# Performance work log

Hardware: AMD Instinct MI355X
Metric: run time of the kernel (lower is better)

The kernel has to match this reference:

```python
import jax, jax.numpy as jnp
import numpy as np

N_NODES = 50000
N_EDGES = 800000
N_REL = 16
N_GRAPHS = 64
IN_DIM = 128
HID = 128
FC = 256
N_CLASSES = 16


def setup_inputs() -> dict:
    key = jax.random.key(0)
    ks = jax.random.split(key, 16)
    h = jax.random.normal(ks[0], (N_NODES, IN_DIM), dtype=jnp.float32)
    src = jax.random.randint(ks[1], (N_EDGES,), 0, N_NODES, dtype=jnp.int32)
    dst = jax.random.randint(ks[2], (N_EDGES,), 0, N_NODES, dtype=jnp.int32)
    rel_types = jax.random.randint(ks[3], (N_EDGES,), 0, N_REL, dtype=jnp.int32)
    graph_ids = jnp.sort(jax.random.randint(ks[4], (N_NODES,), 0, N_GRAPHS, dtype=jnp.int32))
    s1 = 1.0 / np.sqrt(IN_DIM)
    s2 = 1.0 / np.sqrt(HID)
    # RGCN layer 1: per-relation weights, self-loop weight, bias
    W1 = jax.random.normal(ks[5], (N_REL, IN_DIM, HID), dtype=jnp.float32) * s1
    Ws1 = jax.random.normal(ks[6], (IN_DIM, HID), dtype=jnp.float32) * s1
    b1 = jnp.zeros((HID,), dtype=jnp.float32)
    # RGCN layer 2
    W2 = jax.random.normal(ks[7], (N_REL, HID, HID), dtype=jnp.float32) * s2
    Ws2 = jax.random.normal(ks[8], (HID, HID), dtype=jnp.float32) * s2
    b2 = jnp.zeros((HID,), dtype=jnp.float32)
    # FC layer after mean pooling
    Wfc = jax.random.normal(ks[9], (HID, FC), dtype=jnp.float32) * s2
    bfc = jnp.zeros((FC,), dtype=jnp.float32)
    # classify head
    Wc = jax.random.normal(ks[10], (FC, N_CLASSES), dtype=jnp.float32) * (1.0 / np.sqrt(FC))
    bc = jnp.zeros((N_CLASSES,), dtype=jnp.float32)
    return dict(h=h, src=src, dst=dst, rel_types=rel_types, graph_ids=graph_ids,
                W1=W1, Ws1=Ws1, b1=b1, W2=W2, Ws2=Ws2, b2=b2,
                Wfc=Wfc, bfc=bfc, Wc=Wc, bc=bc)


def _rel_graph_conv(h, W, Ws, b, src, dst, rel):
    # dgl RelGraphConv (regularizer=None, self_loop=True, bias=True):
    # out[v] = sum_{e:(u->v)} W[rel_e] @ h[u] + Ws @ h[v] + b
    hW = jnp.einsum('ni,rio->rno', h, W)            # [R, N, out]
    msg = hW[rel, src]                               # [E, out] gather per edge
    agg = jax.ops.segment_sum(msg, dst, num_segments=N_NODES)
    return agg + h @ Ws + b


def _mean_nodes(h, graph_ids):
    sums = jax.ops.segment_sum(h, graph_ids, num_segments=N_GRAPHS)      # [G, D]
    cnts = jax.ops.segment_sum(jnp.ones((h.shape[0], 1), h.dtype), graph_ids,
                               num_segments=N_GRAPHS)                    # [G, 1]
    return sums / jnp.maximum(cnts, 1.0)


def reference(h, src, dst, rel_types, graph_ids,
              W1, Ws1, b1, W2, Ws2, b2, Wfc, bfc, Wc, bc):
    h = h.astype(jnp.float32)
    h = jax.nn.relu(_rel_graph_conv(h, W1, Ws1, b1, src, dst, rel_types))
    h = jax.nn.relu(_rel_graph_conv(h, W2, Ws2, b2, src, dst, rel_types))
    hg = _mean_nodes(h, graph_ids)                   # [G, HID]
    hg = jax.nn.relu(hg @ Wfc + bfc)                 # [G, FC]
    return jax.nn.softmax(hg @ Wc + bc, axis=1)      # [G, n_classes]
```

## Files before the change

kernel.cpp:

```cpp
#include <hip/hip_runtime.h>
#include <hip/hip_bf16.h>

#define N_NODES   50000
#define N_PAD     50048
#define N_EDGES   800000
#define N_REL     16
#define N_GRAPHS  64
#define DIM       128
#define FC_DIM    256
#define N_CLASSES 16

#define SB        50176
#define NBINS_P   (16 * SB)
#define NBLK_PP   784
#define NCOARSE   782
#define NCH       98
#define CHSZ      8192
#define POOL_CH   64
#define MAXBLK_A  13294

#define WS_MARK   0
#define WS_HG     802816
#define WS_CNT    835584
#define WS_SRCOF  835840
#define MEMSET_SZ 4038912
#define WS_BLKH   4038912
#define WS_COFS   4345600
#define WS_PARTP  4348928
#define WS_BLKB   4352256
#define WS_RELB   4355584
#define WS_CIDMAP 4355840
#define WS_RTMP   7567104
#define WS_RECS   10767104
#define WS_OFFSD  13967104
#define WS_X1     14167552
#define WS_X2     26979840
#define WS_AGG    39792128
#define WS_WB     52604416
#define WS_T      53718528

#define XW_TOTAL  (N_PAD * DIM + 2 * 17 * 16384)

typedef __attribute__((ext_vector_type(8))) short bf16x8;
typedef __attribute__((ext_vector_type(4))) float f32x4;

__device__ __forceinline__ void atomAddF(float* p, float v) {
#if defined(__gfx90a__) || defined(__gfx942__) || defined(__gfx950__)
    unsafeAtomicAdd(p, v);
#else
    atomicAdd(p, v);
#endif
}

__device__ __forceinline__ float bf2f(unsigned int u) {
    union { float f; unsigned int i; } x; x.i = u << 16; return x.f;
}
__device__ __forceinline__ unsigned short f2bf(float f) {
    union { float f; unsigned int u; } x; x.f = f;
    unsigned int r = x.u + 0x7fff + ((x.u >> 16) & 1);
    return (unsigned short)(r >> 16);
}
__device__ __forceinline__ void accum8(float* qa, uint4 u) {
    qa[0] += bf2f(u.x & 0xffff); qa[1] += bf2f(u.x >> 16);
    qa[2] += bf2f(u.y & 0xffff); qa[3] += bf2f(u.y >> 16);
    qa[4] += bf2f(u.z & 0xffff); qa[5] += bf2f(u.z >> 16);
    qa[6] += bf2f(u.w & 0xffff); qa[7] += bf2f(u.w >> 16);
}
__device__ __forceinline__ void pack16(const float* qa, unsigned short* dst) {
    #pragma unroll
    for (int j = 0; j < 2; ++j) {
        uint4 w;
        w.x = ((unsigned int)f2bf(qa[j*8+1]) << 16) | f2bf(qa[j*8+0]);
        w.y = ((unsigned int)f2bf(qa[j*8+3]) << 16) | f2bf(qa[j*8+2]);
        w.z = ((unsigned int)f2bf(qa[j*8+5]) << 16) | f2bf(qa[j*8+4]);
        w.w = ((unsigned int)f2bf(qa[j*8+7]) << 16) | f2bf(qa[j*8+6]);
        ((uint4*)dst)[j] = w;
    }
}

__global__ void k_convXW(const float* __restrict__ h, unsigned short* __restrict__ x1,
                         const float* __restrict__ W1, const float* __restrict__ Ws1,
                         const float* __restrict__ W2, const float* __restrict__ Ws2,
                         unsigned short* __restrict__ Wb) {
    int id = blockIdx.x * blockDim.x + threadIdx.x;
    if (id < N_PAD * DIM) {
        int v = id >> 7;
        x1[id] = (v < N_NODES) ? f2bf(h[id]) : (unsigned short)0;
    } else {
        int t = id - N_PAD * DIM;
        int l = t / 278528, rem = t % 278528;
        int r = rem >> 14, rr = rem & 16383;
        int n = rr >> 7, k = rr & 127;
        const float* W  = l ? W2 : W1;
        const float* Ws = l ? Ws2 : Ws1;
        float v = (r < 16) ? W[r * 16384 + k * 128 + n] : Ws[k * 128 + n];
        Wb[t] = f2bf(v);
    }
}

__global__ __launch_bounds__(256) void k_h1(
    const int* __restrict__ src, const int* __restrict__ dst, const int* __restrict__ rel,
    unsigned char* __restrict__ mark, int* __restrict__ blockHist)
{
    __shared__ int hl[NCOARSE];
    int b = blockIdx.x, t = threadIdx.x;
    for (int i = t; i < NCOARSE; i += 256) hl[i] = 0;
    __syncthreads();
    int e0 = b * CHSZ;
    int eend = min(e0 + CHSZ, N_EDGES);
    for (int e = e0 + t; e < eend; e += 256) {
        int d = dst[e];
        mark[rel[e] * SB + src[e]] = 1;
        atomicAdd(&hl[d >> 6], 1);
    }
    __syncthreads();
    for (int i = t; i < NCOARSE; i += 256) blockHist[b * NCOARSE + i] = hl[i];
}

__global__ void k_cscan(int* __restrict__ blockHist, int* __restrict__ coarseOffs) {
    __shared__ int s1[1024], s2[1024];
    int t = threadIdx.x;
    int tot = 0;
    if (t < NCOARSE) {
        int run = 0;
        for (int b = 0; b < NCH; ++b) {
            int v = blockHist[b * NCOARSE + t];
            blockHist[b * NCOARSE + t] = run;
            run += v;
        }
        tot = run;
    }
    s1[t] = tot; __syncthreads();
    int* cur = s1; int* nxt = s2;
    for (int o = 1; o < 1024; o <<= 1) {
        nxt[t] = cur[t] + ((t >= o) ? cur[t - o] : 0);
        __syncthreads();
        int* tmp = cur; cur = nxt; nxt = tmp;
    }
    if (t < NCOARSE) {
        int base = cur[t] - tot;
        coarseOffs[t] = base;
        for (int b = 0; b < NCH; ++b) blockHist[b * NCOARSE + t] += base;
    }
    if (t == NCOARSE) coarseOffs[NCOARSE] = cur[NCOARSE - 1];
}

__global__ void k_scanPA(const unsigned int* __restrict__ markU, int* __restrict__ partP) {
    __shared__ int red[256];
    int b = blockIdx.x, t = threadIdx.x;
    unsigned int u = markU[b * 256 + t];
    red[t] = (int)((u & 1) + ((u >> 8) & 1) + ((u >> 16) & 1) + ((u >> 24) & 1));
    __syncthreads();
    for (int o = 128; o > 0; o >>= 1) {
        if (t < o) red[t] += red[t + o];
        __syncthreads();
    }
    if (t == 0) partP[b] = red[0];
}

__global__ void k_scanPB(const int* __restrict__ partP, int* __restrict__ blkB,
                         int* __restrict__ relB) {
    __shared__ int s1[784], s2[784];
    __shared__ int tot[16], rbase[17];
    int t = threadIdx.x;
    int rel = t / 49, pos = t - rel * 49;
    int v = (t < 784) ? partP[t] : 0;
    if (t < 784) s1[t] = v;
    __syncthreads();
    int* cur = s1; int* nxt = s2;
    for (int o = 1; o < 64; o <<= 1) {
        if (t < 784) nxt[t] = cur[t] + ((pos >= o) ? cur[t - o] : 0);
        __syncthreads();
        int* tmp = cur; cur = nxt; nxt = tmp;
    }
    if (t < 784 && pos == 48) tot[rel] = cur[t];
    __syncthreads();
    if (t == 0) {
        int base = 0;
        for (int r = 0; r < 16; ++r) { rbase[r] = base; base += (tot[r] + 63) & ~63; }
        rbase[16] = base;
    }
    __syncthreads();
    if (t < 784) blkB[t] = rbase[rel] + cur[t] - v;
    if (t < 17)  relB[t] = rbase[t];
}

__global__ void k_scanPC(const unsigned int* __restrict__ markU, const int* __restrict__ blkB,
                         int* __restrict__ cidMap, int* __restrict__ srcOf) {
    __shared__ int s1[256], s2[256];
    int b = blockIdx.x, t = threadIdx.x;
    unsigned int u = markU[b * 256 + t];
    int f0 = (int)(u & 1), f1 = (int)((u >> 8) & 1);
    int f2 = (int)((u >> 16) & 1), f3 = (int)((u >> 24) & 1);
    int sum = f0 + f1 + f2 + f3;
    s1[t] = sum; __syncthreads();
    int* cur = s1; int* nxt = s2;
    for (int o = 1; o < 256; o <<= 1) {
        nxt[t] = cur[t] + ((t >= o) ? cur[t - o] : 0);
        __syncthreads();
        int* tmp = cur; cur = nxt; nxt = tmp;
    }
    int cid = blkB[b] + cur[t] - sum;
    int rel = b / 49;
    int key0 = b * 1024 + t * 4;
    int srcBase = key0 - rel * SB;
    if (f0) { cidMap[key0]     = cid; srcOf[cid] = srcBase;     cid++; }
    if (f1) { cidMap[key0 + 1] = cid; srcOf[cid] = srcBase + 1; cid++; }
    if (f2) { cidMap[key0 + 2] = cid; srcOf[cid] = srcBase + 2; cid++; }
    if (f3) { cidMap[key0 + 3] = cid; srcOf[cid] = srcBase + 3; cid++; }
}

__global__ __launch_bounds__(256) void k_scat1(
    const int* __restrict__ src, const int* __restrict__ dst, const int* __restrict__ rel,
    const int* __restrict__ cidMap, const int* __restrict__ blockHist,
    unsigned int* __restrict__ rtmp)
{
    __shared__ int baseL[NCOARSE];
    __shared__ int hl[NCOARSE];
    int b = blockIdx.x, t = threadIdx.x;
    for (int i = t; i < NCOARSE; i += 256) { baseL[i] = blockHist[b * NCOARSE + i]; hl[i] = 0; }
    __syncthreads();
    int e0 = b * CHSZ;
    int eend = min(e0 + CHSZ, N_EDGES);
    for (int e = e0 + t; e < eend; e += 256) {
        int d = dst[e];
        int cid = cidMap[rel[e] * SB + src[e]];
        int c = d >> 6;
        int rank = atomicAdd(&hl[c], 1);
        rtmp[baseL[c] + rank] = ((unsigned int)cid << 6) | (unsigned int)(d & 63);
    }
}

__global__ __launch_bounds__(256) void k_p2(
    const unsigned int* __restrict__ rtmp, const int* __restrict__ coarseOffs,
    unsigned int* __restrict__ recs, int* __restrict__ offsD)
{
    __shared__ int cntL[64], exclL[65], cur2[64];
    int i = blockIdx.x, t = threadIdx.x;
    int segB = coarseOffs[i], segE = coarseOffs[i + 1];
    if (t < 64) { cntL[t] = 0; cur2[t] = 0; }
    __syncthreads();
    for (int e = segB + t; e < segE; e += 256)
        atomicAdd(&cntL[rtmp[e] & 63u], 1);
    __syncthreads();
    if (t == 0) {
        int run = segB;
        #pragma unroll
        for (int d = 0; d < 64; ++d) { exclL[d] = run; run += cntL[d]; }
        exclL[64] = run;
    }
    __syncthreads();
    if (t < 64) offsD[i * 64 + t] = exclL[t];
    if (t == 64) offsD[i * 64 + 64] = exclL[64];
    for (int e = segB + t; e < segE; e += 256) {
        unsigned int r = rtmp[e];
        int d = (int)(r & 63u);
        int rank = atomicAdd(&cur2[d], 1);
        recs[exclL[d] + rank] = r >> 6;
    }
}

__global__ __launch_bounds__(256) void k_phaseA(
    const unsigned short* __restrict__ x, const unsigned short* __restrict__ Wb,
    const int* __restrict__ srcOf, const int* __restrict__ relB,
    unsigned short* __restrict__ T)
{
    __shared__ unsigned short S[64 * 136];
    __shared__ int sSrc[64];
    __shared__ int sRB[17];

    int tid = threadIdx.x;
    if (tid < 17) sRB[tid] = relB[tid];
    __syncthreads();

    int row0 = blockIdx.x * 64;
    int rtot = sRB[16];
    if (row0 >= rtot + N_PAD) return;

    int r = 16;
    #pragma unroll
    for (int i = 0; i < 16; ++i)
        if (row0 < sRB[i + 1]) { r = i; break; }

    if (tid < 64) sSrc[tid] = (r == 16) ? (row0 - rtot + tid) : srcOf[row0 + tid];
    __syncthreads();

    {
        int row = tid >> 2, c0 = tid & 3;
        const uint4* xp = (const uint4*)(x + (size_t)sSrc[row] * DIM);
        uint4* lp = (uint4*)(&S[row * 136]);
        #pragma unroll
        for (int i = 0; i < 4; ++i) lp[c0 + 4 * i] = xp[c0 + 4 * i];
    }
    __syncthreads();

    int w = tid >> 6, l = tid & 63;
    int nl = l & 15, q = l >> 4;

    f32x4 acc[4][2];
    #pragma unroll
    for (int m = 0; m < 4; ++m) {
        acc[m][0] = (f32x4){0.f, 0.f, 0.f, 0.f};
        acc[m][1] = (f32x4){0.f, 0.f, 0.f, 0.f};
    }

    const unsigned short* wr = Wb + r * 16384;
    #pragma unroll
    for (int kc = 0; kc < 4; ++kc) {
        bf16x8 B0 = *(const bf16x8*)(wr + (w * 32 + nl) * 128 + kc * 32 + q * 8);
        bf16x8 B1 = *(const bf16x8*)(wr + (w * 32 + 16 + nl) * 128 + kc * 32 + q * 8);
        #pragma unroll
        for (int m = 0; m < 4; ++m) {
            bf16x8 a = *(const bf16x8*)(&S[(m * 16 + nl) * 136 + kc * 32 + q * 8]);
            acc[m][0] = __builtin_amdgcn_mfma_f32_16x16x32_bf16(B0, a, acc[m][0], 0, 0, 0);
            acc[m][1] = __builtin_amdgcn_mfma_f32_16x16x32_bf16(B1, a, acc[m][1], 0, 0, 0);
        }
    }
    __syncthreads();
    #pragma unroll
    for (int m = 0; m < 4; ++m) {
        #pragma unroll
        for (int nt = 0; nt < 2; ++nt) {
            uint2 wv;
            wv.x = ((unsigned int)f2bf(acc[m][nt][1]) << 16) | f2bf(acc[m][nt][0]);
            wv.y = ((unsigned int)f2bf(acc[m][nt][3]) << 16) | f2bf(acc[m][nt][2]);
            *(uint2*)(&S[(m * 16 + nl) * 136 + w * 32 + nt * 16 + q * 4]) = wv;
        }
    }
    __syncthreads();
    {
        unsigned short* Tb = T + (size_t)row0 * DIM;
        #pragma unroll
        for (int it = 0; it < 4; ++it) {
            int c = tid + it * 256;
            int row = c >> 4, k8 = c & 15;
            uint4 vv = *(const uint4*)(&S[row * 136 + k8 * 8]);
            *(uint4*)(Tb + row * DIM + k8 * 8) = vv;
        }
    }
}

__global__ __launch_bounds__(256) void k_phaseB(
    const unsigned short* __restrict__ T, const unsigned int* __restrict__ recs,
    const int* __restrict__ offsD, const int* __restrict__ relB,
    const float* __restrict__ bias,
    unsigned short* __restrict__ aggOut, int relu)
{
    __shared__ int sOffs[33];
    __shared__ float sBias[128];
    __shared__ int sSelf;
    int tid = threadIdx.x;
    int v0 = blockIdx.x * 32;
    if (tid < 33) sOffs[tid] = offsD[v0 + tid];
    if (tid == 40) sSelf = relB[16];
    if (tid >= 64 && tid < 96) ((float4*)sBias)[tid - 64] = ((const float4*)bias)[tid - 64];
    __syncthreads();

    int g = tid >> 3, s = tid & 7;
    int dst = v0 + g;
    float qa[16];
    #pragma unroll
    for (int i = 0; i < 16; ++i) qa[i] = sBias[s * 16 + i];

    int beg = sOffs[g], end = sOffs[g + 1];
    int e = beg;
    for (; e + 3 < end; e += 4) {
        unsigned int c0 = recs[e], c1 = recs[e+1], c2 = recs[e+2], c3 = recs[e+3];
        const uint4* t0 = (const uint4*)(T + (size_t)c0 * DIM + s * 16);
        const uint4* t1 = (const uint4*)(T + (size_t)c1 * DIM + s * 16);
        const uint4* t2 = (const uint4*)(T + (size_t)c2 * DIM + s * 16);
        const uint4* t3 = (const uint4*)(T + (size_t)c3 * DIM + s * 16);
        uint4 a0 = t0[0], a1 = t0[1], b0 = t1[0], b1 = t1[1];
        uint4 cc0 = t2[0], cc1 = t2[1], d0 = t3[0], d1 = t3[1];
        accum8(qa, a0); accum8(qa + 8, a1);
        accum8(qa, b0); accum8(qa + 8, b1);
        accum8(qa, cc0); accum8(qa + 8, cc1);
        accum8(qa, d0); accum8(qa + 8, d1);
    }
    for (; e < end; ++e) {
        unsigned int c = recs[e];
        const uint4* tp = (const uint4*)(T + (size_t)c * DIM + s * 16);
        uint4 u0 = tp[0], u1 = tp[1];
        accum8(qa, u0); accum8(qa + 8, u1);
    }
    {
        const uint4* tp = (const uint4*)(T + (size_t)(sSelf + dst) * DIM + s * 16);
        uint4 u0 = tp[0], u1 = tp[1];
        accum8(qa, u0); accum8(qa + 8, u1);
    }

    if (relu) {
        #pragma unroll
        for (int i = 0; i < 16; ++i) qa[i] = fmaxf(qa[i], 0.f);
    }
    pack16(qa, aggOut + (size_t)dst * DIM + s * 16);
}

__global__ void k_pool(const unsigned short* __restrict__ agg2, const int* __restrict__ gids,
                       float* __restrict__ hg_sum, int* __restrict__ cnt)
{
    int d  = threadIdx.x;
    int n0 = blockIdx.x * POOL_CH;
    int nend = min(n0 + POOL_CH, N_NODES);
    if (n0 >= N_NODES) return;
    int curg = gids[n0];
    float run = 0.f;
    for (int n = n0; n < nend; ++n) {
        int g = gids[n];
        if (g != curg) { atomAddF(&hg_sum[curg*DIM + d], run); run = 0.f; curg = g; }
        run += fmaxf(bf2f((unsigned int)agg2[n*DIM + d]), 0.f);
    }
    atomAddF(&hg_sum[curg*DIM + d], run);
    if (d == 0) {
        int cg = gids[n0]; int rl = 0;
        for (int n = n0; n < nend; ++n) {
            int g = gids[n];
            if (g != cg) { atomicAdd(&cnt[cg], rl); rl = 0; cg = g; }
            rl++;
        }
        atomicAdd(&cnt[cg], rl);
    }
}

__global__ __launch_bounds__(256) void k_head(
    const float* __restrict__ hg_sum, const int* __restrict__ cnt,
    const float* __restrict__ Wfc, const float* __restrict__ bfc,
    const float* __restrict__ Wc, const float* __restrict__ bc,
    float* __restrict__ out)
{
    int g = blockIdx.x, t = threadIdx.x;
    __shared__ float hgl[DIM];
    __shared__ float fcl[FC_DIM];
    __shared__ float lg[N_CLASSES];
    if (t < DIM) {
        float c = (float)max(cnt[g], 1);
        hgl[t] = hg_sum[g*DIM + t] / c;
    }
    __syncthreads();
    {
        float sv = bfc[t];
        #pragma unroll 4
        for (int k = 0; k < DIM; ++k) sv += hgl[k] * Wfc[k*FC_DIM + t];
        fcl[t] = fmaxf(sv, 0.f);
    }
    __syncthreads();
    if (t < N_CLASSES) {
        float lgt = bc[t];
        #pragma unroll 4
        for (int k = 0; k < FC_DIM; ++k) lgt += fcl[k] * Wc[k*N_CLASSES + t];
        lg[t] = lgt;
    }
    __syncthreads();
    if (t < N_CLASSES) {
        float m = lg[0];
        #pragma unroll
        for (int c = 1; c < N_CLASSES; ++c) m = fmaxf(m, lg[c]);
        float sden = 0.f;
        #pragma unroll
        for (int c = 0; c < N_CLASSES; ++c) sden += expf(lg[c] - m);
        out[g*N_CLASSES + t] = expf(lg[t] - m) / sden;
    }
}

extern "C" void kernel_launch(void* const* d_in, const int* in_sizes, int n_in,
                              void* d_out, int out_size, void* d_ws, size_t ws_size,
                              hipStream_t stream)
{
    const float* h   = (const float*)d_in[0];
    const int*   src = (const int*)d_in[1];
    const int*   dst = (const int*)d_in[2];
    const int*   rel = (const int*)d_in[3];
    const int*   gid = (const int*)d_in[4];
    const float* W1  = (const float*)d_in[5];
    const float* Ws1 = (const float*)d_in[6];
    const float* b1  = (const float*)d_in[7];
    const float* W2  = (const float*)d_in[8];
    const float* Ws2 = (const float*)d_in[9];
    const float* b2  = (const float*)d_in[10];
    const float* Wfc = (const float*)d_in[11];
    const float* bfc = (const float*)d_in[12];
    const float* Wc  = (const float*)d_in[13];
    const float* bc  = (const float*)d_in[14];
    float* out = (float*)d_out;

    char* ws = (char*)d_ws;
    unsigned char* mark = (unsigned char*)(ws + WS_MARK);
    float* hgsum = (float*)(ws + WS_HG);
    int*   cnt   = (int*)(ws + WS_CNT);
    int*   srcOf = (int*)(ws + WS_SRCOF);
    int*   blkH  = (int*)(ws + WS_BLKH);
    int*   cOffs = (int*)(ws + WS_COFS);
    int*   partP = (int*)(ws + WS_PARTP);
    int*   blkB  = (int*)(ws + WS_BLKB);
    int*   relB  = (int*)(ws + WS_RELB);
    int*   cidMap= (int*)(ws + WS_CIDMAP);
    unsigned int* rtmp = (unsigned int*)(ws + WS_RTMP);
    unsigned int* recs = (unsigned int*)(ws + WS_RECS);
    int*   offsD = (int*)(ws + WS_OFFSD);
    unsigned short* x1  = (unsigned short*)(ws + WS_X1);
    unsigned short* x2  = (unsigned short*)(ws + WS_X2);
    unsigned short* agg = (unsigned short*)(ws + WS_AGG);
    unsigned short* Wb  = (unsigned short*)(ws + WS_WB);
    unsigned short* T   = (unsigned short*)(ws + WS_T);

    int gridA = MAXBLK_A;
    if (ws_size > (size_t)WS_T) {
        long long capRows = (long long)((ws_size - WS_T) / 256);
        long long capBlk = capRows / 64;
        if (capBlk < gridA) gridA = (int)capBlk;
    }

    hipMemsetAsync(mark, 0, MEMSET_SZ, stream);

    k_convXW<<<XW_TOTAL / 256, 256, 0, stream>>>(h, x1, W1, Ws1, W2, Ws2, Wb);
    k_h1<<<NCH, 256, 0, stream>>>(src, dst, rel, mark, blkH);

    k_cscan<<<1, 1024, 0, stream>>>(blkH, cOffs);
    k_scanPA<<<NBLK_PP, 256, 0, stream>>>((const unsigned int*)mark, partP);
    k_scanPB<<<1, 1024, 0, stream>>>(partP, blkB, relB);
    k_scanPC<<<NBLK_PP, 256, 0, stream>>>((const unsigned int*)mark, blkB, cidMap, srcOf);

    k_scat1<<<NCH, 256, 0, stream>>>(src, dst, rel, cidMap, blkH, rtmp);
    k_p2<<<NCOARSE, 256, 0, stream>>>(rtmp, cOffs, recs, offsD);

    k_phaseA<<<gridA, 256, 0, stream>>>(x1, Wb, srcOf, relB, T);
    k_phaseB<<<N_PAD / 32, 256, 0, stream>>>(T, recs, offsD, relB, b1, x2, 1);
    k_phaseA<<<gridA, 256, 0, stream>>>(x2, Wb + 17 * 16384, srcOf, relB, T);
    k_phaseB<<<N_PAD / 32, 256, 0, stream>>>(T, recs, offsD, relB, b2, agg, 0);

    k_pool<<<(N_PAD + POOL_CH - 1) / POOL_CH, 128, 0, stream>>>(agg, gid, hgsum, cnt);
    k_head<<<N_GRAPHS, 256, 0, stream>>>(hgsum, cnt, Wfc, bfc, Wc, bc, out);
}
```

Baseline: 454.9 us.

## Aggregate-then-transform RGCN: sort edges by (dst, rel) and fuse gather with MFMA

Drops the transform-then-gather scheme, which built a compacted (rel, src) table and materialised per-relation transformed rows T. The new version buckets edges by destination bin and by (local dst, rel), sums raw bf16 source features per relation into shared memory, then runs one 64x128x128 MFMA per relation plus one for the self loop in a single fused kernel. It also merges the histogram pass with the input and weight conversion, and splits the coarse scan into a parallel column scan plus a small final scan. This removes the mark/cidMap scans, the large T buffer and the separate phase B pass. In exchange each block runs 17 serialized gather-plus-GEMM rounds with two barriers each, has only 782 blocks, and load is uneven across relations and destinations.

```diff
diff --git a/kernel.cpp b/kernel.cpp
--- a/kernel.cpp
+++ b/kernel.cpp
@@ -10,36 +10,26 @@
 #define FC_DIM    256
 #define N_CLASSES 16
 
-#define SB        50176
-#define NBINS_P   (16 * SB)
-#define NBLK_PP   784
 #define NCOARSE   782
-#define NCH       98
-#define CHSZ      8192
+#define NCH       196
+#define CHSZ      4096
 #define POOL_CH   64
-#define MAXBLK_A  13294
-
-#define WS_MARK   0
-#define WS_HG     802816
-#define WS_CNT    835584
-#define WS_SRCOF  835840
-#define MEMSET_SZ 4038912
-#define WS_BLKH   4038912
-#define WS_COFS   4345600
-#define WS_PARTP  4348928
-#define WS_BLKB   4352256
-#define WS_RELB   4355584
-#define WS_CIDMAP 4355840
-#define WS_RTMP   7567104
-#define WS_RECS   10767104
-#define WS_OFFSD  13967104
-#define WS_X1     14167552
-#define WS_X2     26979840
-#define WS_AGG    39792128
-#define WS_WB     52604416
-#define WS_T      53718528
-
+
+#define NBLK_CX   27200
 #define XW_TOTAL  (N_PAD * DIM + 2 * 17 * 16384)
+
+#define WS_HG     0
+#define WS_CNT    32768
+#define MEMSET_SZ 33024
+#define WS_BLKH   33024
+#define WS_COFS   646400
+#define WS_RTMP   649728
+#define WS_RECS   3849728
+#define WS_OFFSDR 7049728
+#define WS_X1     10253056
+#define WS_X2     23065344
+#define WS_AGG    35877632
+#define WS_WB     48689920
 
 typedef __attribute__((ext_vector_type(8))) short bf16x8;
 typedef __attribute__((ext_vector_type(4))) float f32x4;
@@ -78,224 +68,155 @@
     }
 }
 
-__global__ void k_convXW(const float* __restrict__ h, unsigned short* __restrict__ x1,
-                         const float* __restrict__ W1, const float* __restrict__ Ws1,
-                         const float* __restrict__ W2, const float* __restrict__ Ws2,
-                         unsigned short* __restrict__ Wb) {
-    int id = blockIdx.x * blockDim.x + threadIdx.x;
-    if (id < N_PAD * DIM) {
-        int v = id >> 7;
-        x1[id] = (v < N_NODES) ? f2bf(h[id]) : (unsigned short)0;
+__global__ __launch_bounds__(256) void k_h1cx(
+    const int* __restrict__ dst,
+    int* __restrict__ blockHist,
+    const float* __restrict__ h, unsigned short* __restrict__ x1,
+    const float* __restrict__ W1, const float* __restrict__ Ws1,
+    const float* __restrict__ W2, const float* __restrict__ Ws2,
+    unsigned short* __restrict__ Wb)
+{
+    __shared__ int hl[NCOARSE];
+    int t = threadIdx.x;
+    if (blockIdx.x < NCH) {
+        int b = blockIdx.x;
+        for (int i = t; i < NCOARSE; i += 256) hl[i] = 0;
+        __syncthreads();
+        int e0 = b * CHSZ;
+        int eend = min(e0 + CHSZ, N_EDGES);
+        for (int e = e0 + t; e < eend; e += 256)
+            atomicAdd(&hl[dst[e] >> 6], 1);
+        __syncthreads();
+        for (int i = t; i < NCOARSE; i += 256) blockHist[b * NCOARSE + i] = hl[i];
     } else {
-        int t = id - N_PAD * DIM;
-        int l = t / 278528, rem = t % 278528;
-        int r = rem >> 14, rr = rem & 16383;
-        int n = rr >> 7, k = rr & 127;
-        const float* W  = l ? W2 : W1;
-        const float* Ws = l ? Ws2 : Ws1;
-        float v = (r < 16) ? W[r * 16384 + k * 128 + n] : Ws[k * 128 + n];
-        Wb[t] = f2bf(v);
-    }
-}
-
-__global__ __launch_bounds__(256) void k_h1(
+        int id = (blockIdx.x - NCH) * 256 + t;
+        if (id < N_PAD * DIM) {
+            int v = id >> 7;
+            x1[id] = (v < N_NODES) ? f2bf(h[id]) : (unsigned short)0;
+        } else {
+            int tt = id - N_PAD * DIM;
+            int l = tt / 278528, rem = tt % 278528;
+            int r = rem >> 14, rr = rem & 16383;
+            int n = rr >> 7, k = rr & 127;
+            const float* W  = l ? W2 : W1;
+            const float* Ws = l ? Ws2 : Ws1;
+            float v = (r < 16) ? W[r * 16384 + k * 128 + n] : Ws[k * 128 + n];
+            Wb[tt] = f2bf(v);
+        }
+    }
+}
+
+__global__ __launch_bounds__(256) void k_csA(int* __restrict__ blockHist,
+                                             int* __restrict__ cOffs)
+{
+    __shared__ int sc[2][256];
+    int i = blockIdx.x, t = threadIdx.x;
+    int v = (t < NCH) ? blockHist[t * NCOARSE + i] : 0;
+    sc[0][t] = v; __syncthreads();
+    int cur = 0;
+    for (int o = 1; o < 256; o <<= 1) {
+        sc[cur ^ 1][t] = sc[cur][t] + ((t >= o) ? sc[cur][t - o] : 0);
+        __syncthreads();
+        cur ^= 1;
+    }
+    if (t < NCH) blockHist[t * NCOARSE + i] = sc[cur][t] - v;
+    if (t == NCH - 1) cOffs[i] = sc[cur][t];
+}
+
+__global__ __launch_bounds__(1024) void k_csB(int* __restrict__ cOffs)
+{
+    __shared__ int c1[1024], c2[1024];
+    int t = threadIdx.x;
+    int v = (t < NCOARSE) ? cOffs[t] : 0;
+    c1[t] = v; __syncthreads();
+    int* cur = c1; int* nxt = c2;
+    for (int o = 1; o < 1024; o <<= 1) {
+        nxt[t] = cur[t] + ((t >= o) ? cur[t - o] : 0);
+        __syncthreads();
+        int* tmp = cur; cur = nxt; nxt = tmp;
+    }
+    if (t < NCOARSE) cOffs[t] = cur[t] - v;
+    if (t == NCOARSE) cOffs[NCOARSE] = cur[NCOARSE - 1];
+}
+
+__global__ __launch_bounds__(256) void k_scat1(
     const int* __restrict__ src, const int* __restrict__ dst, const int* __restrict__ rel,
-    unsigned char* __restrict__ mark, int* __restrict__ blockHist)
-{
+    const int* __restrict__ blockHist, const int* __restrict__ cOffs,
+    unsigned int* __restrict__ rtmp)
+{
+    __shared__ int baseL[NCOARSE];
     __shared__ int hl[NCOARSE];
     int b = blockIdx.x, t = threadIdx.x;
-    for (int i = t; i < NCOARSE; i += 256) hl[i] = 0;
+    for (int i = t; i < NCOARSE; i += 256) {
+        baseL[i] = blockHist[b * NCOARSE + i] + cOffs[i];
+        hl[i] = 0;
+    }
     __syncthreads();
     int e0 = b * CHSZ;
     int eend = min(e0 + CHSZ, N_EDGES);
     for (int e = e0 + t; e < eend; e += 256) {
         int d = dst[e];
-        mark[rel[e] * SB + src[e]] = 1;
-        atomicAdd(&hl[d >> 6], 1);
-    }
-    __syncthreads();
-    for (int i = t; i < NCOARSE; i += 256) blockHist[b * NCOARSE + i] = hl[i];
-}
-
-__global__ void k_cscan(int* __restrict__ blockHist, int* __restrict__ coarseOffs) {
-    __shared__ int s1[1024], s2[1024];
-    int t = threadIdx.x;
-    int tot = 0;
-    if (t < NCOARSE) {
-        int run = 0;
-        for (int b = 0; b < NCH; ++b) {
-            int v = blockHist[b * NCOARSE + t];
-            blockHist[b * NCOARSE + t] = run;
-            run += v;
-        }
-        tot = run;
-    }
-    s1[t] = tot; __syncthreads();
-    int* cur = s1; int* nxt = s2;
-    for (int o = 1; o < 1024; o <<= 1) {
-        nxt[t] = cur[t] + ((t >= o) ? cur[t - o] : 0);
-        __syncthreads();
-        int* tmp = cur; cur = nxt; nxt = tmp;
-    }
-    if (t < NCOARSE) {
-        int base = cur[t] - tot;
-        coarseOffs[t] = base;
-        for (int b = 0; b < NCH; ++b) blockHist[b * NCOARSE + t] += base;
-    }
-    if (t == NCOARSE) coarseOffs[NCOARSE] = cur[NCOARSE - 1];
-}
-
-__global__ void k_scanPA(const unsigned int* __restrict__ markU, int* __restrict__ partP) {
-    __shared__ int red[256];
-    int b = blockIdx.x, t = threadIdx.x;
-    unsigned int u = markU[b * 256 + t];
-    red[t] = (int)((u & 1) + ((u >> 8) & 1) + ((u >> 16) & 1) + ((u >> 24) & 1));
-    __syncthreads();
-    for (int o = 128; o > 0; o >>= 1) {
-        if (t < o) red[t] += red[t + o];
-        __syncthreads();
-    }
-    if (t == 0) partP[b] = red[0];
-}
-
-__global__ void k_scanPB(const int* __restrict__ partP, int* __restrict__ blkB,
-                         int* __restrict__ relB) {
-    __shared__ int s1[784], s2[784];
-    __shared__ int tot[16], rbase[17];
-    int t = threadIdx.x;
-    int rel = t / 49, pos = t - rel * 49;
-    int v = (t < 784) ? partP[t] : 0;
-    if (t < 784) s1[t] = v;
-    __syncthreads();
-    int* cur = s1; int* nxt = s2;
-    for (int o = 1; o < 64; o <<= 1) {
-        if (t < 784) nxt[t] = cur[t] + ((pos >= o) ? cur[t - o] : 0);
-        __syncthreads();
-        int* tmp = cur; cur = nxt; nxt = tmp;
-    }
-    if (t < 784 && pos == 48) tot[rel] = cur[t];
-    __syncthreads();
-    if (t == 0) {
-        int base = 0;
-        for (int r = 0; r < 16; ++r) { rbase[r] = base; base += (tot[r] + 63) & ~63; }
-        rbase[16] = base;
-    }
-    __syncthreads();
-    if (t < 784) blkB[t] = rbase[rel] + cur[t] - v;
-    if (t < 17)  relB[t] = rbase[t];
-}
-
-__global__ void k_scanPC(const unsigned int* __restrict__ markU, const int* __restrict__ blkB,
-                         int* __restrict__ cidMap, int* __restrict__ srcOf) {
-    __shared__ int s1[256], s2[256];
-    int b = blockIdx.x, t = threadIdx.x;
-    unsigned int u = markU[b * 256 + t];
-    int f0 = (int)(u & 1), f1 = (int)((u >> 8) & 1);
-    int f2 = (int)((u >> 16) & 1), f3 = (int)((u >> 24) & 1);
-    int sum = f0 + f1 + f2 + f3;
-    s1[t] = sum; __syncthreads();
-    int* cur = s1; int* nxt = s2;
+        int c = d >> 6;
+        int rank = atomicAdd(&hl[c], 1);
+        rtmp[baseL[c] + rank] = ((unsigned int)src[e] << 10)
+                              | ((unsigned int)(d & 63) << 4)
+                              | (unsigned int)rel[e];
+    }
+}
+
+__global__ __launch_bounds__(256) void k_p2(
+    const unsigned int* __restrict__ rtmp, const int* __restrict__ cOffs,
+    unsigned int* __restrict__ recs, int* __restrict__ offsDR)
+{
+    __shared__ int cnt[1024];
+    __shared__ int part[256], part2[256];
+    int i = blockIdx.x, t = threadIdx.x;
+    int segB = cOffs[i], segE = cOffs[i + 1];
+    for (int k = t; k < 1024; k += 256) cnt[k] = 0;
+    __syncthreads();
+    for (int e = segB + t; e < segE; e += 256)
+        atomicAdd(&cnt[rtmp[e] & 1023u], 1);
+    __syncthreads();
+    int b4 = t * 4;
+    int s0 = cnt[b4], s1 = cnt[b4+1], s2 = cnt[b4+2], s3 = cnt[b4+3];
+    int tsum = s0 + s1 + s2 + s3;
+    part[t] = tsum;
+    __syncthreads();
+    int* cur = part; int* nxt = part2;
     for (int o = 1; o < 256; o <<= 1) {
         nxt[t] = cur[t] + ((t >= o) ? cur[t - o] : 0);
         __syncthreads();
         int* tmp = cur; cur = nxt; nxt = tmp;
     }
-    int cid = blkB[b] + cur[t] - sum;
-    int rel = b / 49;
-    int key0 = b * 1024 + t * 4;
-    int srcBase = key0 - rel * SB;
-    if (f0) { cidMap[key0]     = cid; srcOf[cid] = srcBase;     cid++; }
-    if (f1) { cidMap[key0 + 1] = cid; srcOf[cid] = srcBase + 1; cid++; }
-    if (f2) { cidMap[key0 + 2] = cid; srcOf[cid] = srcBase + 2; cid++; }
-    if (f3) { cidMap[key0 + 3] = cid; srcOf[cid] = srcBase + 3; cid++; }
-}
-
-__global__ __launch_bounds__(256) void k_scat1(
-    const int* __restrict__ src, const int* __restrict__ dst, const int* __restrict__ rel,
-    const int* __restrict__ cidMap, const int* __restrict__ blockHist,
-    unsigned int* __restrict__ rtmp)
-{
-    __shared__ int baseL[NCOARSE];
-    __shared__ int hl[NCOARSE];
-    int b = blockIdx.x, t = threadIdx.x;
-    for (int i = t; i < NCOARSE; i += 256) { baseL[i] = blockHist[b * NCOARSE + i]; hl[i] = 0; }
-    __syncthreads();
-    int e0 = b * CHSZ;
-    int eend = min(e0 + CHSZ, N_EDGES);
-    for (int e = e0 + t; e < eend; e += 256) {
-        int d = dst[e];
-        int cid = cidMap[rel[e] * SB + src[e]];
-        int c = d >> 6;
-        int rank = atomicAdd(&hl[c], 1);
-        rtmp[baseL[c] + rank] = ((unsigned int)cid << 6) | (unsigned int)(d & 63);
-    }
-}
-
-__global__ __launch_bounds__(256) void k_p2(
-    const unsigned int* __restrict__ rtmp, const int* __restrict__ coarseOffs,
-    unsigned int* __restrict__ recs, int* __restrict__ offsD)
-{
-    __shared__ int cntL[64], exclL[65], cur2[64];
-    int i = blockIdx.x, t = threadIdx.x;
-    int segB = coarseOffs[i], segE = coarseOffs[i + 1];
-    if (t < 64) { cntL[t] = 0; cur2[t] = 0; }
-    __syncthreads();
-    for (int e = segB + t; e < segE; e += 256)
-        atomicAdd(&cntL[rtmp[e] & 63u], 1);
-    __syncthreads();
-    if (t == 0) {
-        int run = segB;
-        #pragma unroll
-        for (int d = 0; d < 64; ++d) { exclL[d] = run; run += cntL[d]; }
-        exclL[64] = run;
-    }
-    __syncthreads();
-    if (t < 64) offsD[i * 64 + t] = exclL[t];
-    if (t == 64) offsD[i * 64 + 64] = exclL[64];
+    int excl = cur[t] - tsum + segB;
+    cnt[b4]     = excl;
+    cnt[b4 + 1] = excl + s0;
+    cnt[b4 + 2] = excl + s0 + s1;
+    cnt[b4 + 3] = excl + s0 + s1 + s2;
+    __syncthreads();
+    for (int k = t; k < 1024; k += 256) offsDR[i * 1024 + k] = cnt[k];
+    if (i == NCOARSE - 1 && t == 0) offsDR[NCOARSE * 1024] = segE;
     for (int e = segB + t; e < segE; e += 256) {
         unsigned int r = rtmp[e];
-        int d = (int)(r & 63u);
-        int rank = atomicAdd(&cur2[d], 1);
-        recs[exclL[d] + rank] = r >> 6;
-    }
-}
-
-__global__ __launch_bounds__(256) void k_phaseA(
+        int pos = atomicAdd(&cnt[r & 1023u], 1);
+        recs[pos] = r >> 10;
+    }
+}
+
+__global__ __launch_bounds__(256) void k_rgcn(
     const unsigned short* __restrict__ x, const unsigned short* __restrict__ Wb,
-    const int* __restrict__ srcOf, const int* __restrict__ relB,
-    unsigned short* __restrict__ T)
-{
-    __shared__ unsigned short S[64 * 136];
-    __shared__ int sSrc[64];
-    __shared__ int sRB[17];
-
+    const unsigned int* __restrict__ recs, const int* __restrict__ offsDR,
+    const float* __restrict__ bias, unsigned short* __restrict__ out, int relu)
+{
+    __shared__ __attribute__((aligned(16))) unsigned short S[64 * 136];
+    __shared__ int sOffs[1025];
     int tid = threadIdx.x;
-    if (tid < 17) sRB[tid] = relB[tid];
-    __syncthreads();
-
-    int row0 = blockIdx.x * 64;
-    int rtot = sRB[16];
-    if (row0 >= rtot + N_PAD) return;
-
-    int r = 16;
-    #pragma unroll
-    for (int i = 0; i < 16; ++i)
-        if (row0 < sRB[i + 1]) { r = i; break; }
-
-    if (tid < 64) sSrc[tid] = (r == 16) ? (row0 - rtot + tid) : srcOf[row0 + tid];
-    __syncthreads();
-
-    {
-        int row = tid >> 2, c0 = tid & 3;
-        const uint4* xp = (const uint4*)(x + (size_t)sSrc[row] * DIM);
-        uint4* lp = (uint4*)(&S[row * 136]);
-        #pragma unroll
-        for (int i = 0; i < 4; ++i) lp[c0 + 4 * i] = xp[c0 + 4 * i];
-    }
-    __syncthreads();
-
-    int w = tid >> 6, l = tid & 63;
-    int nl = l & 15, q = l >> 4;
+    int bin = blockIdx.x;
+    int v0 = bin * 64;
+    for (int k = tid; k < 1025; k += 256) sOffs[k] = offsDR[bin * 1024 + k];
+
+    int w = tid >> 6, l = tid & 63, nl = l & 15, q = l >> 4;
+    int gh = tid >> 3, s = tid & 7;
 
     f32x4 acc[4][2];
     #pragma unroll
@@ -303,97 +224,69 @@
         acc[m][0] = (f32x4){0.f, 0.f, 0.f, 0.f};
         acc[m][1] = (f32x4){0.f, 0.f, 0.f, 0.f};
     }
-
-    const unsigned short* wr = Wb + r * 16384;
-    #pragma unroll
-    for (int kc = 0; kc < 4; ++kc) {
-        bf16x8 B0 = *(const bf16x8*)(wr + (w * 32 + nl) * 128 + kc * 32 + q * 8);
-        bf16x8 B1 = *(const bf16x8*)(wr + (w * 32 + 16 + nl) * 128 + kc * 32 + q * 8);
-        #pragma unroll
-        for (int m = 0; m < 4; ++m) {
-            bf16x8 a = *(const bf16x8*)(&S[(m * 16 + nl) * 136 + kc * 32 + q * 8]);
-            acc[m][0] = __builtin_amdgcn_mfma_f32_16x16x32_bf16(B0, a, acc[m][0], 0, 0, 0);
-            acc[m][1] = __builtin_amdgcn_mfma_f32_16x16x32_bf16(B1, a, acc[m][1], 0, 0, 0);
-        }
-    }
-    __syncthreads();
+    __syncthreads();
+
+    for (int r = 0; r < 17; ++r) {
+        #pragma unroll
+        for (int hf = 0; hf < 2; ++hf) {
+            int g = hf * 32 + gh;
+            float qa[16];
+            #pragma unroll
+            for (int j = 0; j < 16; ++j) qa[j] = 0.f;
+            if (r == 16) {
+                const uint4* xp = (const uint4*)(x + (size_t)(v0 + g) * DIM + s * 16);
+                uint4 u0 = xp[0], u1 = xp[1];
+                accum8(qa, u0); accum8(qa + 8, u1);
+            } else {
+                int o0 = sOffs[g * 16 + r], o1 = sOffs[g * 16 + r + 1];
+                for (int e = o0; e < o1; ++e) {
+                    const uint4* xp = (const uint4*)(x + (size_t)recs[e] * DIM + s * 16);
+                    uint4 u0 = xp[0], u1 = xp[1];
+                    accum8(qa, u0); accum8(qa + 8, u1);
+                }
+            }
+            pack16(qa, &S[g * 136 + s * 16]);
+        }
+        __syncthreads();
+        const unsigned short* wr = Wb + r * 16384;
+        #pragma unroll
+        for (int kc = 0; kc < 4; ++kc) {
+            bf16x8 b0 = *(const bf16x8*)(wr + (w * 32 + nl) * 128 + kc * 32 + q * 8);
+            bf16x8 b1 = *(const bf16x8*)(wr + (w * 32 + 16 + nl) * 128 + kc * 32 + q * 8);
+            #pragma unroll
+            for (int m = 0; m < 4; ++m) {
+                bf16x8 a = *(const bf16x8*)(&S[(m * 16 + nl) * 136 + kc * 32 + q * 8]);
+                acc[m][0] = __builtin_amdgcn_mfma_f32_16x16x32_bf16(a, b0, acc[m][0], 0, 0, 0);
+                acc[m][1] = __builtin_amdgcn_mfma_f32_16x16x32_bf16(a, b1, acc[m][1], 0, 0, 0);
+            }
+        }
+        __syncthreads();
+    }
+
+    float bv0 = bias[w * 32 + nl], bv1 = bias[w * 32 + 16 + nl];
     #pragma unroll
     for (int m = 0; m < 4; ++m) {
         #pragma unroll
-        for (int nt = 0; nt < 2; ++nt) {
-            uint2 wv;
-            wv.x = ((unsigned int)f2bf(acc[m][nt][1]) << 16) | f2bf(acc[m][nt][0]);
-            wv.y = ((unsigned int)f2bf(acc[m][nt][3]) << 16) | f2bf(acc[m][nt][2]);
-            *(uint2*)(&S[(m * 16 + nl) * 136 + w * 32 + nt * 16 + q * 4]) = wv;
+        for (int reg = 0; reg < 4; ++reg) {
+            int row = m * 16 + q * 4 + reg;
+            float f0 = acc[m][0][reg] + bv0;
+            float f1 = acc[m][1][reg] + bv1;
+            if (relu) { f0 = fmaxf(f0, 0.f); f1 = fmaxf(f1, 0.f); }
+            S[row * 136 + (w * 32 + nl)]      = f2bf(f0);
+            S[row * 136 + (w * 32 + 16 + nl)] = f2bf(f1);
         }
     }
     __syncthreads();
     {
-        unsigned short* Tb = T + (size_t)row0 * DIM;
+        unsigned short* Ob = out + (size_t)v0 * DIM;
         #pragma unroll
         for (int it = 0; it < 4; ++it) {
             int c = tid + it * 256;
-            int row = c >> 4, k8 = c & 15;
-            uint4 vv = *(const uint4*)(&S[row * 136 + k8 * 8]);
-            *(uint4*)(Tb + row * DIM + k8 * 8) = vv;
-        }
-    }
-}
-
-__global__ __launch_bounds__(256) void k_phaseB(
-    const unsigned short* __restrict__ T, const unsigned int* __restrict__ recs,
-    const int* __restrict__ offsD, const int* __restrict__ relB,
-    const float* __restrict__ bias,
-    unsigned short* __restrict__ aggOut, int relu)
-{
-    __shared__ int sOffs[33];
-    __shared__ float sBias[128];
-    __shared__ int sSelf;
-    int tid = threadIdx.x;
-    int v0 = blockIdx.x * 32;
-    if (tid < 33) sOffs[tid] = offsD[v0 + tid];
-    if (tid == 40) sSelf = relB[16];
-    if (tid >= 64 && tid < 96) ((float4*)sBias)[tid - 64] = ((const float4*)bias)[tid - 64];
-    __syncthreads();
-
-    int g = tid >> 3, s = tid & 7;
-    int dst = v0 + g;
-    float qa[16];
-    #pragma unroll
-    for (int i = 0; i < 16; ++i) qa[i] = sBias[s * 16 + i];
-
-    int beg = sOffs[g], end = sOffs[g + 1];
-    int e = beg;
-    for (; e + 3 < end; e += 4) {
-        unsigned int c0 = recs[e], c1 = recs[e+1], c2 = recs[e+2], c3 = recs[e+3];
-        const uint4* t0 = (const uint4*)(T + (size_t)c0 * DIM + s * 16);
-        const uint4* t1 = (const uint4*)(T + (size_t)c1 * DIM + s * 16);
-        const uint4* t2 = (const uint4*)(T + (size_t)c2 * DIM + s * 16);
-        const uint4* t3 = (const uint4*)(T + (size_t)c3 * DIM + s * 16);
-        uint4 a0 = t0[0], a1 = t0[1], b0 = t1[0], b1 = t1[1];
-        uint4 cc0 = t2[0], cc1 = t2[1], d0 = t3[0], d1 = t3[1];
-        accum8(qa, a0); accum8(qa + 8, a1);
-        accum8(qa, b0); accum8(qa + 8, b1);
-        accum8(qa, cc0); accum8(qa + 8, cc1);
-        accum8(qa, d0); accum8(qa + 8, d1);
-    }
-    for (; e < end; ++e) {
-        unsigned int c = recs[e];
-        const uint4* tp = (const uint4*)(T + (size_t)c * DIM + s * 16);
-        uint4 u0 = tp[0], u1 = tp[1];
-        accum8(qa, u0); accum8(qa + 8, u1);
-    }
-    {
-        const uint4* tp = (const uint4*)(T + (size_t)(sSelf + dst) * DIM + s * 16);
-        uint4 u0 = tp[0], u1 = tp[1];
-        accum8(qa, u0); accum8(qa + 8, u1);
-    }
-
-    if (relu) {
-        #pragma unroll
-        for (int i = 0; i < 16; ++i) qa[i] = fmaxf(qa[i], 0.f);
-    }
-    pack16(qa, aggOut + (size_t)dst * DIM + s * 16);
+            int rw = c >> 4, k8 = c & 15;
+            uint4 vv = *(const uint4*)(&S[rw * 136 + k8 * 8]);
+            *(uint4*)(Ob + rw * DIM + k8 * 8) = vv;
+        }
+    }
 }
 
 __global__ void k_pool(const unsigned short* __restrict__ agg2, const int* __restrict__ gids,
@@ -484,49 +377,28 @@
     float* out = (float*)d_out;
 
     char* ws = (char*)d_ws;
-    unsigned char* mark = (unsigned char*)(ws + WS_MARK);
     float* hgsum = (float*)(ws + WS_HG);
     int*   cnt   = (int*)(ws + WS_CNT);
-    int*   srcOf = (int*)(ws + WS_SRCOF);
     int*   blkH  = (int*)(ws + WS_BLKH);
     int*   cOffs = (int*)(ws + WS_COFS);
-    int*   partP = (int*)(ws + WS_PARTP);
-    int*   blkB  = (int*)(ws + WS_BLKB);
-    int*   relB  = (int*)(ws + WS_RELB);
-    int*   cidMap= (int*)(ws + WS_CIDMAP);
     unsigned int* rtmp = (unsigned int*)(ws + WS_RTMP);
     unsigned int* recs = (unsigned int*)(ws + WS_RECS);
-    int*   offsD = (int*)(ws + WS_OFFSD);
+    int*   offsDR = (int*)(ws + WS_OFFSDR);
     unsigned short* x1  = (unsigned short*)(ws + WS_X1);
     unsigned short* x2  = (unsigned short*)(ws + WS_X2);
     unsigned short* agg = (unsigned short*)(ws + WS_AGG);
     unsigned short* Wb  = (unsigned short*)(ws + WS_WB);
-    unsigned short* T   = (unsigned short*)(ws + WS_T);
-
-    int gridA = MAXBLK_A;
-    if (ws_size > (size_t)WS_T) {
-        long long capRows = (long long)((ws_size - WS_T) / 256);
-        long long capBlk = capRows / 64;
-        if (capBlk < gridA) gridA = (int)capBlk;
-    }
-
-    hipMemsetAsync(mark, 0, MEMSET_SZ, stream);
-
-    k_convXW<<<XW_TOTAL / 256, 256, 0, stream>>>(h, x1, W1, Ws1, W2, Ws2, Wb);
-    k_h1<<<NCH, 256, 0, stream>>>(src, dst, rel, mark, blkH);
-
-    k_cscan<<<1, 1024, 0, stream>>>(blkH, cOffs);
-    k_scanPA<<<NBLK_PP, 256, 0, stream>>>((const unsigned int*)mark, partP);
-    k_scanPB<<<1, 1024, 0, stream>>>(partP, blkB, relB);
-    k_scanPC<<<NBLK_PP, 256, 0, stream>>>((const unsigned int*)mark, blkB, cidMap, srcOf);
-
-    k_scat1<<<NCH, 256, 0, stream>>>(src, dst, rel, cidMap, blkH, rtmp);
-    k_p2<<<NCOARSE, 256, 0, stream>>>(rtmp, cOffs, recs, offsD);
-
-    k_phaseA<<<gridA, 256, 0, stream>>>(x1, Wb, srcOf, relB, T);
-    k_phaseB<<<N_PAD / 32, 256, 0, stream>>>(T, recs, offsD, relB, b1, x2, 1);
-    k_phaseA<<<gridA, 256, 0, stream>>>(x2, Wb + 17 * 16384, srcOf, relB, T);
-    k_phaseB<<<N_PAD / 32, 256, 0, stream>>>(T, recs, offsD, relB, b2, agg, 0);
+
+    hipMemsetAsync(ws + WS_HG, 0, MEMSET_SZ, stream);
+
+    k_h1cx<<<NCH + NBLK_CX, 256, 0, stream>>>(dst, blkH, h, x1, W1, Ws1, W2, Ws2, Wb);
+    k_csA<<<NCOARSE, 256, 0, stream>>>(blkH, cOffs);
+    k_csB<<<1, 1024, 0, stream>>>(cOffs);
+    k_scat1<<<NCH, 256, 0, stream>>>(src, dst, rel, blkH, cOffs, rtmp);
+    k_p2<<<NCOARSE, 256, 0, stream>>>(rtmp, cOffs, recs, offsDR);
+
+    k_rgcn<<<NCOARSE, 256, 0, stream>>>(x1, Wb, recs, offsDR, b1, x2, 1);
+    k_rgcn<<<NCOARSE, 256, 0, stream>>>(x2, Wb + 17 * 16384, recs, offsDR, b2, agg, 0);
 
     k_pool<<<(N_PAD + POOL_CH - 1) / POOL_CH, 128, 0, stream>>>(agg, gid, hgsum, cnt);
     k_head<<<N_GRAPHS, 256, 0, stream>>>(hgsum, cnt, Wfc, bfc, Wc, bc, out);
```

Measured after the change: 449.0 us. Within noise of the previous version (-1.3%).
